# Optimization experiments

Hardware: AMD Instinct MI355X
Metric: run time of the kernel (lower is better)

The kernel has to match this reference:

```python
import jax, jax.numpy as jnp
import numpy as np

D_MODEL = 1024
N_HEADS = 16
HEAD_DIM = D_MODEL // N_HEADS  # 64


def setup_inputs() -> dict:
    key = jax.random.key(0)
    k1, k2, k3 = jax.random.split(key, 3)
    x = jax.random.normal(k1, (2, 2048, D_MODEL), dtype=jnp.float32)
    # nn.Linear(d, 3d, bias=False): store transposed so y = x @ W
    w_qkv = jax.random.normal(k2, (D_MODEL, 3 * D_MODEL), dtype=jnp.float32) * (D_MODEL ** -0.5)
    w_proj = jax.random.normal(k3, (D_MODEL, D_MODEL), dtype=jnp.float32) * (D_MODEL ** -0.5)
    return {"x": x, "w_qkv": w_qkv, "w_proj": w_proj}


def reference(x, w_qkv, w_proj):
    b, n, _ = x.shape
    qkv = x @ w_qkv  # [b, n, 3*d_model]
    # einops 'b n (h d qkv) -> qkv b h n d': qkv axis is innermost of the split
    qkv = qkv.reshape(b, n, N_HEADS, HEAD_DIM, 3)
    q = jnp.moveaxis(qkv[..., 0], 1, 2)  # [b, h, n, d]
    k = jnp.moveaxis(qkv[..., 1], 1, 2)
    v = jnp.moveaxis(qkv[..., 2], 1, 2)
    scale = HEAD_DIM ** -0.5
    scores = jnp.einsum('bhqd,bhkd->bhqk', q, k) * scale  # [b, h, n, n]
    causal = jnp.tril(jnp.ones((n, n), dtype=bool))
    scores = jnp.where(causal[None, None], scores, -jnp.inf)
    attn = jax.nn.softmax(scores, axis=-1)
    out = jnp.einsum('bhqk,bhkd->bhqd', attn, v)  # [b, h, n, d]
    out = jnp.moveaxis(out, 1, 2).reshape(b, n, D_MODEL)  # 'b h n d -> b n (h d)'
    return out @ w_proj
```

## Files before the change

### kernel.cpp

```cpp
#include <hip/hip_runtime.h>
#include <cstdint>
#include <cstddef>

#define D_MODEL 1024
#define N_HEADS 16
#define HEAD_DIM 64
#define SEQ 2048
#define BATCH 2

typedef __attribute__((ext_vector_type(8))) short bf16x8;
typedef __attribute__((ext_vector_type(4))) float f32x4;

__device__ inline unsigned short f2bf(float f) {
    union { float f; unsigned u; } v; v.f = f;
    unsigned r = v.u + 0x7fffu + ((v.u >> 16) & 1u);
    return (unsigned short)(r >> 16);
}

__device__ __forceinline__ void gload_lds16(const unsigned short* g, unsigned short* l) {
    __builtin_amdgcn_global_load_lds(
        (const __attribute__((address_space(1))) unsigned int*)g,
        (__attribute__((address_space(3))) unsigned int*)l, 16, 0, 0);
}

__global__ __launch_bounds__(256) void convert_x_kernel(
    const float* __restrict__ X, unsigned short* __restrict__ Xb)
{
    const int idx = blockIdx.x * 256 + threadIdx.x;
    const float4* src = (const float4*)X;
    float4 v0 = src[idx * 2], v1 = src[idx * 2 + 1];
    union { unsigned short u[8]; uint4 v; } o;
    o.u[0] = f2bf(v0.x); o.u[1] = f2bf(v0.y); o.u[2] = f2bf(v0.z); o.u[3] = f2bf(v0.w);
    o.u[4] = f2bf(v1.x); o.u[5] = f2bf(v1.y); o.u[6] = f2bf(v1.z); o.u[7] = f2bf(v1.w);
    ((uint4*)Xb)[idx] = o.v;
}

__global__ __launch_bounds__(256) void convert_transpose_qkv(
    const float* __restrict__ W, unsigned short* __restrict__ Wt)
{
    __shared__ float t[32][33];
    const int c0 = blockIdx.x * 32, r0 = blockIdx.y * 32;
    const int a = threadIdx.x & 31, b = threadIdx.x >> 5;
#pragma unroll
    for (int i = 0; i < 32; i += 8)
        t[b + i][a] = W[(size_t)(r0 + b + i) * (3 * D_MODEL) + c0 + a];
    __syncthreads();
#pragma unroll
    for (int i = 0; i < 32; i += 8) {
        const int c = c0 + b + i;
        const int np = (c % 3) * 1024 + c / 3;
        Wt[(size_t)np * D_MODEL + r0 + a] = f2bf(t[a][b + i]);
    }
}

__global__ __launch_bounds__(256) void convert_transpose_kernel(
    const float* __restrict__ W, unsigned short* __restrict__ Wt,
    int ncols, int nrows)
{
    __shared__ float t[32][33];
    const int c0 = blockIdx.x * 32, r0 = blockIdx.y * 32;
    const int a = threadIdx.x & 31, b = threadIdx.x >> 5;
#pragma unroll
    for (int i = 0; i < 32; i += 8)
        t[b + i][a] = W[(size_t)(r0 + b + i) * ncols + c0 + a];
    __syncthreads();
#pragma unroll
    for (int i = 0; i < 32; i += 8)
        Wt[(size_t)(c0 + b + i) * nrows + r0 + a] = f2bf(t[a][b + i]);
}

__global__ __launch_bounds__(256) void v_transpose(
    const unsigned short* __restrict__ V, unsigned short* __restrict__ Vt)
{
    const int n0 = blockIdx.x * 64;
    const int bh = blockIdx.y;
    __shared__ unsigned short t[64 * 72];
    const int tid = threadIdx.x;
    const uint4* src = (const uint4*)(V + ((size_t)bh * SEQ + n0) * HEAD_DIM);
#pragma unroll
    for (int it = 0; it < 2; it++) {
        const int lin = tid + it * 256;
        const int row = lin >> 3, p = lin & 7;
        ((uint4*)t)[row * 9 + p] = src[lin];
    }
    __syncthreads();
#pragma unroll
    for (int it = 0; it < 2; it++) {
        const int lin = tid + it * 256;
        const int drow = lin >> 3, p = lin & 7;
        union { unsigned short u[8]; uint4 v; } o;
#pragma unroll
        for (int e = 0; e < 8; e++) o.u[e] = t[(p * 8 + e) * 72 + drow];
        ((uint4*)(Vt + ((size_t)bh * HEAD_DIM + drow) * SEQ + n0))[p] = o.v;
    }
}

__global__ __launch_bounds__(512) void gemm_qkv_mfma(
    const unsigned short* __restrict__ A, const unsigned short* __restrict__ B,
    unsigned short* __restrict__ Q, unsigned short* __restrict__ Kq,
    unsigned short* __restrict__ Vb)
{
    const int tid = threadIdx.x;
    const int w = tid >> 6, lane = tid & 63;
    const int l15 = lane & 15, quad = lane >> 4;
    const int wr = w >> 2, wc = w & 3;
    const int row0 = blockIdx.y * 128, col0 = blockIdx.x * 256;

    __shared__ unsigned short As[2][4096];
    __shared__ unsigned short Bs[2][8192];

    const f32x4 zero4 = {0.f, 0.f, 0.f, 0.f};
    f32x4 acc[4][4];
#pragma unroll
    for (int i = 0; i < 4; i++)
#pragma unroll
        for (int j = 0; j < 4; j++) acc[i][j] = zero4;

    auto stage_ = [&](int sb, int k0) {
#pragma unroll
        for (int i = 0; i < 3; i++) {
            const int f = w * 3 + i;
            if (f < 8) {
                gload_lds16(A + (size_t)(row0 + f * 16 + l15) * D_MODEL + k0 + quad * 8,
                            &As[sb][f * 512 + lane * 8]);
            } else {
                const int fn = f - 8;
                gload_lds16(B + (size_t)(col0 + fn * 16 + l15) * D_MODEL + k0 + quad * 8,
                            &Bs[sb][fn * 512 + lane * 8]);
            }
        }
    };

    stage_(0, 0);
    for (int kt = 0; kt < 32; kt++) {
        const int sb = kt & 1;
        __syncthreads();
        if (kt + 1 < 32) stage_(sb ^ 1, (kt + 1) * 32);
        bf16x8 af[4], bfr[4];
#pragma unroll
        for (int i = 0; i < 4; i++)
            af[i] = *(const bf16x8*)&As[sb][(wr * 4 + i) * 512 + lane * 8];
#pragma unroll
        for (int j = 0; j < 4; j++)
            bfr[j] = *(const bf16x8*)&Bs[sb][(wc * 4 + j) * 512 + lane * 8];
#pragma unroll
        for (int i = 0; i < 4; i++)
#pragma unroll
            for (int j = 0; j < 4; j++)
                acc[i][j] = __builtin_amdgcn_mfma_f32_16x16x32_bf16(
                    af[i], bfr[j], acc[i][j], 0, 0, 0);
    }

    const int nbase = col0 + wc * 64;
    const int which = nbase >> 10;
    unsigned short* const dst = (which == 0) ? Q : (which == 1) ? Kq : Vb;
#pragma unroll
    for (int i = 0; i < 4; i++) {
#pragma unroll
        for (int r = 0; r < 4; r++) {
            const int row = row0 + wr * 64 + i * 16 + quad * 4 + r;
            const int bb = row >> 11, n = row & (SEQ - 1);
#pragma unroll
            for (int j = 0; j < 4; j++) {
                const int idx = (nbase + j * 16 + l15) & 1023;
                const int h = idx >> 6, dd = idx & 63;
                dst[(((size_t)(bb * N_HEADS + h)) * SEQ + n) * HEAD_DIM + dd] =
                    f2bf(acc[i][j][r]);
            }
        }
    }
}

__global__ __launch_bounds__(256) void gemm_proj_mfma(
    const unsigned short* __restrict__ A, const unsigned short* __restrict__ B,
    float* __restrict__ C)
{
    const int tid = threadIdx.x;
    const int w = tid >> 6, lane = tid & 63;
    const int l15 = lane & 15, quad = lane >> 4;
    const int wr = w >> 1, wc = w & 1;
    const int row0 = blockIdx.y * 128, col0 = blockIdx.x * 128;

    __shared__ unsigned short As[2][4096];
    __shared__ unsigned short Bs[2][4096];

    const f32x4 zero4 = {0.f, 0.f, 0.f, 0.f};
    f32x4 acc[4][4];
#pragma unroll
    for (int i = 0; i < 4; i++)
#pragma unroll
        for (int j = 0; j < 4; j++) acc[i][j] = zero4;

    auto stage_ = [&](int sb, int k0) {
#pragma unroll
        for (int i = 0; i < 2; i++) {
            const int f = w * 2 + i;
            gload_lds16(A + (size_t)(row0 + f * 16 + l15) * D_MODEL + k0 + quad * 8,
                        &As[sb][f * 512 + lane * 8]);
            gload_lds16(B + (size_t)(col0 + f * 16 + l15) * D_MODEL + k0 + quad * 8,
                        &Bs[sb][f * 512 + lane * 8]);
        }
    };

    stage_(0, 0);
    for (int kt = 0; kt < 32; kt++) {
        const int sb = kt & 1;
        __syncthreads();
        if (kt + 1 < 32) stage_(sb ^ 1, (kt + 1) * 32);
        bf16x8 af[4], bfr[4];
#pragma unroll
        for (int i = 0; i < 4; i++)
            af[i] = *(const bf16x8*)&As[sb][(wr * 4 + i) * 512 + lane * 8];
#pragma unroll
        for (int j = 0; j < 4; j++)
            bfr[j] = *(const bf16x8*)&Bs[sb][(wc * 4 + j) * 512 + lane * 8];
#pragma unroll
        for (int i = 0; i < 4; i++)
#pragma unroll
            for (int j = 0; j < 4; j++)
                acc[i][j] = __builtin_amdgcn_mfma_f32_16x16x32_bf16(
                    af[i], bfr[j], acc[i][j], 0, 0, 0);
    }

#pragma unroll
    for (int i = 0; i < 4; i++) {
#pragma unroll
        for (int r = 0; r < 4; r++) {
            const int row = row0 + wr * 64 + i * 16 + quad * 4 + r;
#pragma unroll
            for (int j = 0; j < 4; j++) {
                const int c = col0 + wc * 64 + j * 16 + l15;
                C[(size_t)row * D_MODEL + c] = acc[i][j][r];
            }
        }
    }
}

#define PSTR 72

__global__ __launch_bounds__(256) void flash_attn_kernel(
    const unsigned short* __restrict__ Q,
    const unsigned short* __restrict__ K,
    const unsigned short* __restrict__ Vt,
    unsigned short* __restrict__ O)
{
    const int idx = blockIdx.x;
    const int bh = idx & 31;
    const int qt2 = idx >> 5;
    const int hi = qt2 >> 3, lo = qt2 & 7;
    const int qt = (hi == 0) ? lo : (hi == 1) ? 31 - lo : (hi == 2) ? lo + 8 : 23 - lo;

    const int tid = threadIdx.x;
    const int w = tid >> 6, lane = tid & 63;
    const int l15 = lane & 15, quad = lane >> 4;

    __shared__ unsigned short Ks[2][4096];
    __shared__ unsigned short Vs[2][4096];
    __shared__ unsigned short Ps[4][16 * PSTR];

    bf16x8 qf[2];
    {
        const unsigned short* qrow =
            Q + ((size_t)bh * SEQ + qt * 64 + w * 16 + l15) * HEAD_DIM;
        qf[0] = *(const bf16x8*)(qrow + quad * 8);
        qf[1] = *(const bf16x8*)(qrow + 32 + quad * 8);
    }

    const f32x4 zero4 = {0.f, 0.f, 0.f, 0.f};
    f32x4 o_acc[4] = {zero4, zero4, zero4, zero4};
    float m_i = -1e30f, l_i = 0.f;

    auto stage = [&](int bf, int kt_t) {
        const int key0 = kt_t * 64;
#pragma unroll
        for (int i = 0; i < 2; i++) {
            const int f = w * 2 + i;
            const int ct = f >> 1, kh = f & 1;
            gload_lds16(K + ((size_t)bh * SEQ + key0 + ct * 16 + l15) * HEAD_DIM
                          + kh * 32 + quad * 8,
                        &Ks[bf][f * 512 + lane * 8]);
            gload_lds16(Vt + ((size_t)bh * HEAD_DIM + ct * 16 + l15) * SEQ
                           + key0 + kh * 32 + quad * 8,
                        &Vs[bf][f * 512 + lane * 8]);
        }
    };

    stage(0, 0);
    int buf = 0;

    const int qg = qt * 64 + w * 16 + l15;

    for (int kt = 0; kt <= qt; kt++) {
        __syncthreads();
        if (kt < qt) stage(buf ^ 1, kt + 1);

        f32x4 st[4] = {zero4, zero4, zero4, zero4};
#pragma unroll
        for (int kh = 0; kh < 2; kh++) {
#pragma unroll
            for (int ct = 0; ct < 4; ct++) {
                bf16x8 kf = *(const bf16x8*)&Ks[buf][(ct * 2 + kh) * 512 + lane * 8];
                st[ct] = __builtin_amdgcn_mfma_f32_16x16x32_bf16(kf, qf[kh], st[ct], 0, 0, 0);
            }
        }

        const bool diag = (kt == qt);
        float mt = -1e30f;
#pragma unroll
        for (int ct = 0; ct < 4; ct++) {
#pragma unroll
            for (int r = 0; r < 4; r++) {
                float v = st[ct][r] * 0.125f;
                const int kg = kt * 64 + ct * 16 + quad * 4 + r;
                if (diag && kg > qg) v = -1e30f;
                st[ct][r] = v;
                mt = fmaxf(mt, v);
            }
        }
        mt = fmaxf(mt, __shfl_xor(mt, 16));
        mt = fmaxf(mt, __shfl_xor(mt, 32));

        const float mn = fmaxf(m_i, mt);
        const float alpha = __expf(m_i - mn);
        m_i = mn;

        float ls = 0.f;
#pragma unroll
        for (int ct = 0; ct < 4; ct++) {
            union { unsigned short u[4]; uint2 v; } pk;
#pragma unroll
            for (int r = 0; r < 4; r++) {
                float p = __expf(st[ct][r] - mn);
                ls += p;
                pk.u[r] = f2bf(p);
            }
            *(uint2*)&Ps[w][l15 * PSTR + ct * 16 + quad * 4] = pk.v;
        }
        ls += __shfl_xor(ls, 16);
        ls += __shfl_xor(ls, 32);
        l_i = l_i * alpha + ls;

        float ar[4];
#pragma unroll
        for (int r = 0; r < 4; r++)
            ar[r] = __shfl(alpha, (lane & 48) | (quad * 4 + r));
#pragma unroll
        for (int dt = 0; dt < 4; dt++)
#pragma unroll
            for (int r = 0; r < 4; r++)
                o_acc[dt][r] *= ar[r];

#pragma unroll
        for (int kh = 0; kh < 2; kh++) {
            bf16x8 pa = *(const bf16x8*)&Ps[w][l15 * PSTR + kh * 32 + quad * 8];
#pragma unroll
            for (int dt = 0; dt < 4; dt++) {
                bf16x8 vf = *(const bf16x8*)&Vs[buf][(dt * 2 + kh) * 512 + lane * 8];
                o_acc[dt] = __builtin_amdgcn_mfma_f32_16x16x32_bf16(pa, vf, o_acc[dt], 0, 0, 0);
            }
        }
        buf ^= 1;
    }

    const float linv = 1.0f / l_i;
    float lr[4];
#pragma unroll
    for (int r = 0; r < 4; r++)
        lr[r] = __shfl(linv, (lane & 48) | (quad * 4 + r));

    const int b = bh >> 4, h = bh & 15;
#pragma unroll
    for (int r = 0; r < 4; r++) {
        const int q = qt * 64 + w * 16 + quad * 4 + r;
        unsigned short* orow = O + ((size_t)b * SEQ + q) * D_MODEL + h * HEAD_DIM;
#pragma unroll
        for (int dt = 0; dt < 4; dt++)
            orow[dt * 16 + l15] = f2bf(o_acc[dt][r] * lr[r]);
    }
}

extern "C" void kernel_launch(void* const* d_in, const int* in_sizes, int n_in,
                              void* d_out, int out_size, void* d_ws, size_t ws_size,
                              hipStream_t stream) {
    const float* x      = (const float*)d_in[0];
    const float* w_qkv  = (const float*)d_in[1];
    const float* w_proj = (const float*)d_in[2];
    float* out = (float*)d_out;

    unsigned short* Xb  = (unsigned short*)d_ws;
    unsigned short* Wqt = Xb  + (size_t)4 * 1024 * 1024;
    unsigned short* Wpt = Wqt + (size_t)3 * 1024 * 1024;
    unsigned short* Qb  = Wpt + (size_t)1 * 1024 * 1024;
    unsigned short* Kb  = Qb  + (size_t)4 * 1024 * 1024;
    unsigned short* Vb  = Kb  + (size_t)4 * 1024 * 1024;
    unsigned short* Vtb = Vb  + (size_t)4 * 1024 * 1024;
    unsigned short* Ob  = Vtb + (size_t)4 * 1024 * 1024;

    convert_x_kernel<<<dim3(2048), 256, 0, stream>>>(x, Xb);
    convert_transpose_qkv<<<dim3(3072 / 32, 1024 / 32), 256, 0, stream>>>(w_qkv, Wqt);
    convert_transpose_kernel<<<dim3(1024 / 32, 1024 / 32), 256, 0, stream>>>(
        w_proj, Wpt, D_MODEL, D_MODEL);

    gemm_qkv_mfma<<<dim3(3 * D_MODEL / 256, BATCH * SEQ / 128), 512, 0, stream>>>(
        Xb, Wqt, Qb, Kb, Vb);

    v_transpose<<<dim3(SEQ / 64, BATCH * N_HEADS), 256, 0, stream>>>(Vb, Vtb);

    flash_attn_kernel<<<dim3(SEQ / 64 * BATCH * N_HEADS), 256, 0, stream>>>(
        Qb, Kb, Vtb, Ob);

    gemm_proj_mfma<<<dim3(D_MODEL / 128, BATCH * SEQ / 128), 256, 0, stream>>>(
        Ob, Wpt, out);
}
```

Measured before the change: 239.0 us.

## Fuse conversion kernels into one launch and split-K the output projection

Three separate fp32-to-bf16 conversion and transpose kernels become one launch that dispatches on block index. The output projection GEMM is split over K into two halves with a BK=64 tile, which doubles the grid from 256 to 512 blocks. The two fp32 partial results go into the reused Q/K workspace, and a new kernel adds them into the output. This should improve occupancy on the many CUs and cut launch overhead, at the cost of extra partial-sum memory traffic and one more launch.

```diff
diff --git a/kernel.cpp b/kernel.cpp
--- a/kernel.cpp
+++ b/kernel.cpp
@@ -23,50 +23,49 @@
         (__attribute__((address_space(3))) unsigned int*)l, 16, 0, 0);
 }
 
-__global__ __launch_bounds__(256) void convert_x_kernel(
-    const float* __restrict__ X, unsigned short* __restrict__ Xb)
-{
-    const int idx = blockIdx.x * 256 + threadIdx.x;
-    const float4* src = (const float4*)X;
-    float4 v0 = src[idx * 2], v1 = src[idx * 2 + 1];
-    union { unsigned short u[8]; uint4 v; } o;
-    o.u[0] = f2bf(v0.x); o.u[1] = f2bf(v0.y); o.u[2] = f2bf(v0.z); o.u[3] = f2bf(v0.w);
-    o.u[4] = f2bf(v1.x); o.u[5] = f2bf(v1.y); o.u[6] = f2bf(v1.z); o.u[7] = f2bf(v1.w);
-    ((uint4*)Xb)[idx] = o.v;
-}
-
-__global__ __launch_bounds__(256) void convert_transpose_qkv(
-    const float* __restrict__ W, unsigned short* __restrict__ Wt)
-{
+__global__ __launch_bounds__(256) void fused_convert_kernel(
+    const float* __restrict__ X, unsigned short* __restrict__ Xb,
+    const float* __restrict__ Wq, unsigned short* __restrict__ Wqt,
+    const float* __restrict__ Wp, unsigned short* __restrict__ Wpt)
+{
+    const int blk = blockIdx.x;
+    const int tid = threadIdx.x;
     __shared__ float t[32][33];
-    const int c0 = blockIdx.x * 32, r0 = blockIdx.y * 32;
-    const int a = threadIdx.x & 31, b = threadIdx.x >> 5;
-#pragma unroll
-    for (int i = 0; i < 32; i += 8)
-        t[b + i][a] = W[(size_t)(r0 + b + i) * (3 * D_MODEL) + c0 + a];
-    __syncthreads();
-#pragma unroll
-    for (int i = 0; i < 32; i += 8) {
-        const int c = c0 + b + i;
-        const int np = (c % 3) * 1024 + c / 3;
-        Wt[(size_t)np * D_MODEL + r0 + a] = f2bf(t[a][b + i]);
-    }
-}
-
-__global__ __launch_bounds__(256) void convert_transpose_kernel(
-    const float* __restrict__ W, unsigned short* __restrict__ Wt,
-    int ncols, int nrows)
-{
-    __shared__ float t[32][33];
-    const int c0 = blockIdx.x * 32, r0 = blockIdx.y * 32;
-    const int a = threadIdx.x & 31, b = threadIdx.x >> 5;
-#pragma unroll
-    for (int i = 0; i < 32; i += 8)
-        t[b + i][a] = W[(size_t)(r0 + b + i) * ncols + c0 + a];
-    __syncthreads();
-#pragma unroll
-    for (int i = 0; i < 32; i += 8)
-        Wt[(size_t)(c0 + b + i) * nrows + r0 + a] = f2bf(t[a][b + i]);
+
+    if (blk < 2048) {
+        const int idx = blk * 256 + tid;
+        const float4* src = (const float4*)X;
+        float4 v0 = src[idx * 2], v1 = src[idx * 2 + 1];
+        union { unsigned short u[8]; uint4 v; } o;
+        o.u[0] = f2bf(v0.x); o.u[1] = f2bf(v0.y); o.u[2] = f2bf(v0.z); o.u[3] = f2bf(v0.w);
+        o.u[4] = f2bf(v1.x); o.u[5] = f2bf(v1.y); o.u[6] = f2bf(v1.z); o.u[7] = f2bf(v1.w);
+        ((uint4*)Xb)[idx] = o.v;
+    } else if (blk < 5120) {
+        const int bb = blk - 2048;
+        const int c0 = (bb % 96) * 32, r0 = (bb / 96) * 32;
+        const int a = tid & 31, b = tid >> 5;
+#pragma unroll
+        for (int i = 0; i < 32; i += 8)
+            t[b + i][a] = Wq[(size_t)(r0 + b + i) * (3 * D_MODEL) + c0 + a];
+        __syncthreads();
+#pragma unroll
+        for (int i = 0; i < 32; i += 8) {
+            const int c = c0 + b + i;
+            const int np = (c % 3) * 1024 + c / 3;
+            Wqt[(size_t)np * D_MODEL + r0 + a] = f2bf(t[a][b + i]);
+        }
+    } else {
+        const int bb = blk - 5120;
+        const int c0 = (bb % 32) * 32, r0 = (bb / 32) * 32;
+        const int a = tid & 31, b = tid >> 5;
+#pragma unroll
+        for (int i = 0; i < 32; i += 8)
+            t[b + i][a] = Wp[(size_t)(r0 + b + i) * D_MODEL + c0 + a];
+        __syncthreads();
+#pragma unroll
+        for (int i = 0; i < 32; i += 8)
+            Wpt[(size_t)(c0 + b + i) * D_MODEL + r0 + a] = f2bf(t[a][b + i]);
+    }
 }
 
 __global__ __launch_bounds__(256) void v_transpose(
@@ -171,18 +170,19 @@
     }
 }
 
-__global__ __launch_bounds__(256) void gemm_proj_mfma(
+__global__ __launch_bounds__(256) void gemm_proj_splitk(
     const unsigned short* __restrict__ A, const unsigned short* __restrict__ B,
-    float* __restrict__ C)
+    float* __restrict__ P)
 {
     const int tid = threadIdx.x;
     const int w = tid >> 6, lane = tid & 63;
     const int l15 = lane & 15, quad = lane >> 4;
     const int wr = w >> 1, wc = w & 1;
     const int row0 = blockIdx.y * 128, col0 = blockIdx.x * 128;
-
-    __shared__ unsigned short As[2][4096];
-    __shared__ unsigned short Bs[2][4096];
+    const int kbase = blockIdx.z * 512;
+
+    __shared__ unsigned short As[2][8192];
+    __shared__ unsigned short Bs[2][8192];
 
     const f32x4 zero4 = {0.f, 0.f, 0.f, 0.f};
     f32x4 acc[4][4];
@@ -193,35 +193,41 @@
 
     auto stage_ = [&](int sb, int k0) {
 #pragma unroll
-        for (int i = 0; i < 2; i++) {
-            const int f = w * 2 + i;
-            gload_lds16(A + (size_t)(row0 + f * 16 + l15) * D_MODEL + k0 + quad * 8,
-                        &As[sb][f * 512 + lane * 8]);
-            gload_lds16(B + (size_t)(col0 + f * 16 + l15) * D_MODEL + k0 + quad * 8,
-                        &Bs[sb][f * 512 + lane * 8]);
+        for (int i = 0; i < 4; i++) {
+            const int fa = w * 4 + i;
+            const int mt = fa >> 1, kh = fa & 1;
+            const int kc = kbase + k0 + kh * 32 + quad * 8;
+            gload_lds16(A + (size_t)(row0 + mt * 16 + l15) * D_MODEL + kc,
+                        &As[sb][fa * 512 + lane * 8]);
+            gload_lds16(B + (size_t)(col0 + mt * 16 + l15) * D_MODEL + kc,
+                        &Bs[sb][fa * 512 + lane * 8]);
         }
     };
 
     stage_(0, 0);
-    for (int kt = 0; kt < 32; kt++) {
+    for (int kt = 0; kt < 8; kt++) {
         const int sb = kt & 1;
         __syncthreads();
-        if (kt + 1 < 32) stage_(sb ^ 1, (kt + 1) * 32);
-        bf16x8 af[4], bfr[4];
-#pragma unroll
-        for (int i = 0; i < 4; i++)
-            af[i] = *(const bf16x8*)&As[sb][(wr * 4 + i) * 512 + lane * 8];
-#pragma unroll
-        for (int j = 0; j < 4; j++)
-            bfr[j] = *(const bf16x8*)&Bs[sb][(wc * 4 + j) * 512 + lane * 8];
-#pragma unroll
-        for (int i = 0; i < 4; i++)
+        if (kt + 1 < 8) stage_(sb ^ 1, (kt + 1) * 64);
+#pragma unroll
+        for (int kh = 0; kh < 2; kh++) {
+            bf16x8 af[4], bfr[4];
+#pragma unroll
+            for (int i = 0; i < 4; i++)
+                af[i] = *(const bf16x8*)&As[sb][((wr * 4 + i) * 2 + kh) * 512 + lane * 8];
 #pragma unroll
             for (int j = 0; j < 4; j++)
-                acc[i][j] = __builtin_amdgcn_mfma_f32_16x16x32_bf16(
-                    af[i], bfr[j], acc[i][j], 0, 0, 0);
-    }
-
+                bfr[j] = *(const bf16x8*)&Bs[sb][((wc * 4 + j) * 2 + kh) * 512 + lane * 8];
+#pragma unroll
+            for (int i = 0; i < 4; i++)
+#pragma unroll
+                for (int j = 0; j < 4; j++)
+                    acc[i][j] = __builtin_amdgcn_mfma_f32_16x16x32_bf16(
+                        af[i], bfr[j], acc[i][j], 0, 0, 0);
+        }
+    }
+
+    float* const dst = P + (size_t)blockIdx.z * (4096ull * 1024ull);
 #pragma unroll
     for (int i = 0; i < 4; i++) {
 #pragma unroll
@@ -230,9 +236,24 @@
 #pragma unroll
             for (int j = 0; j < 4; j++) {
                 const int c = col0 + wc * 64 + j * 16 + l15;
-                C[(size_t)row * D_MODEL + c] = acc[i][j][r];
-            }
-        }
+                dst[(size_t)row * D_MODEL + c] = acc[i][j][r];
+            }
+        }
+    }
+}
+
+__global__ __launch_bounds__(256) void add_out_kernel(
+    const float* __restrict__ P, float* __restrict__ out)
+{
+    const float4* p0 = (const float4*)P;
+    const float4* p1 = (const float4*)(P + 4096ull * 1024ull);
+    float4* o = (float4*)out;
+    const int base = (blockIdx.x * 256 + threadIdx.x) * 4;
+#pragma unroll
+    for (int j = 0; j < 4; j++) {
+        float4 a = p0[base + j], b = p1[base + j];
+        float4 r = {a.x + b.x, a.y + b.y, a.z + b.z, a.w + b.w};
+        o[base + j] = r;
     }
 }
 
@@ -396,10 +417,10 @@
     unsigned short* Vtb = Vb  + (size_t)4 * 1024 * 1024;
     unsigned short* Ob  = Vtb + (size_t)4 * 1024 * 1024;
 
-    convert_x_kernel<<<dim3(2048), 256, 0, stream>>>(x, Xb);
-    convert_transpose_qkv<<<dim3(3072 / 32, 1024 / 32), 256, 0, stream>>>(w_qkv, Wqt);
-    convert_transpose_kernel<<<dim3(1024 / 32, 1024 / 32), 256, 0, stream>>>(
-        w_proj, Wpt, D_MODEL, D_MODEL);
+    float* Pp = (float*)Qb;
+
+    fused_convert_kernel<<<dim3(6144), 256, 0, stream>>>(
+        x, Xb, w_qkv, Wqt, w_proj, Wpt);
 
     gemm_qkv_mfma<<<dim3(3 * D_MODEL / 256, BATCH * SEQ / 128), 512, 0, stream>>>(
         Xb, Wqt, Qb, Kb, Vb);
@@ -409,6 +430,8 @@
     flash_attn_kernel<<<dim3(SEQ / 64 * BATCH * N_HEADS), 256, 0, stream>>>(
         Qb, Kb, Vtb, Ob);
 
-    gemm_proj_mfma<<<dim3(D_MODEL / 128, BATCH * SEQ / 128), 256, 0, stream>>>(
-        Ob, Wpt, out);
-}
+    gemm_proj_splitk<<<dim3(D_MODEL / 128, BATCH * SEQ / 128, 2), 256, 0, stream>>>(
+        Ob, Wpt, Pp);
+
+    add_out_kernel<<<dim3(1024), 256, 0, stream>>>(Pp, out);
+}
```

Result: no change. 234.6 us (-1.9%).
